# Kernel tuning notes

Hardware: AMD Instinct MI355X
Metric: run time of the kernel (lower is better)

The kernel has to match this reference:

```python
import jax, jax.numpy as jnp
import numpy as np
from jax import lax

B, T, H, L, V = 64, 512, 1024, 4, 32000


def setup_inputs() -> dict:
    key = jax.random.key(0)
    ks = jax.random.split(key, 8)
    lengths = jax.random.randint(ks[0], (B,), T // 2, T + 1)
    tok = jax.random.randint(ks[1], (B, T), 1, V)  # valid tokens are >0; 0 is pad
    x = jnp.where(jnp.arange(T)[None, :] < lengths[:, None], tok, 0)
    s = float(1.0 / np.sqrt(H))  # torch LSTMCell default init bound
    emb = jax.random.normal(ks[2], (V, H), jnp.float32) * 0.02
    W_ih = jax.random.uniform(ks[3], (L, 4 * H, H), jnp.float32, -s, s)
    W_hh = jax.random.uniform(ks[4], (L, 4 * H, H), jnp.float32, -s, s)
    b_ih = jax.random.uniform(ks[5], (L, 4 * H), jnp.float32, -s, s)
    b_hh = jax.random.uniform(ks[6], (L, 4 * H), jnp.float32, -s, s)
    h0 = jnp.zeros((L, B, H), jnp.float32)
    c0 = jnp.zeros((L, B, H), jnp.float32)
    return {"x": x, "h0": h0, "c0": c0, "emb": emb,
            "W_ih": W_ih, "W_hh": W_hh, "b_ih": b_ih, "b_hh": b_hh}


def _lstm_stack_step(h, c, xt, W_ih, W_hh, b_ih, b_hh):
    # h, c: [L, B, H]; xt: [B, H]. Every layer is H->H (module quirk).
    inp = xt
    new_h, new_c = [], []
    for l in range(L):
        gates = inp @ W_ih[l].T + b_ih[l] + h[l] @ W_hh[l].T + b_hh[l]  # [B, 4H]
        i, f, g, o = jnp.split(gates, 4, axis=-1)  # torch gate order i,f,g,o
        i = jax.nn.sigmoid(i)
        f = jax.nn.sigmoid(f)
        g = jnp.tanh(g)
        o = jax.nn.sigmoid(o)
        cl = f * c[l] + i * g
        hl = o * jnp.tanh(cl)
        new_h.append(hl)
        new_c.append(cl)
        inp = hl
    return jnp.stack(new_h), jnp.stack(new_c)


def reference(x, h0, c0, emb, W_ih, W_hh, b_ih, b_hh):
    # lengths from pad-token convention (pad id = 0)
    lengths = jnp.sum(x > 0, axis=1)  # [B]
    # pack(..., enforce_sorted=False): sort sequences by length, descending.
    order = jnp.argsort(-lengths)          # stable descending sort
    inv = jnp.argsort(order)               # to unsort the padded output
    xs = x[order]                          # [B, T] sorted order
    lens = lengths[order]                  # [B]
    e = emb[xs]                            # [B, T, H] embedded
    mask = jnp.arange(T)[None, :] < lens[:, None]  # [B, T] active-at-step

    def step(carry, inp):
        h, c = carry                       # [L, B, H] each
        xt, m = inp                        # xt: [B, H], m: [B] bool
        nh, nc = _lstm_stack_step(h, c, xt, W_ih, W_hh, b_ih, b_hh)
        m3 = m[None, :, None]
        h2 = jnp.where(m3, nh, h)          # only active (prefix) rows advance
        c2 = jnp.where(m3, nc, c)
        out = jnp.where(m[:, None], nh[L - 1], 0.0)  # unpack zero-pads
        return (h2, c2), out

    (hF, cF), outs = lax.scan(step, (h0, c0),
                              (jnp.swapaxes(e, 0, 1), mask.T))  # scan over T
    output = jnp.swapaxes(outs, 0, 1)[inv]  # [B, T, H] back to original order
    # NOTE: the torch module returns `state` indexed in SORTED order (it never
    # unsorts the state buffer); we reproduce that quirk faithfully.
    return output, hF, cF
```

## Files before the change

### kernel.cpp

```cpp
#include <hip/hip_runtime.h>
#include <hip/hip_bf16.h>
#include <stdint.h>

#define Bn 64
#define Tn 512
#define Hn 1024
#define Ln 4
#define GN 4096
#define NDIAG (Tn + Ln - 1)
#define LBH (Ln * Bn * Hn)

typedef __attribute__((ext_vector_type(8))) short bf16x8;
typedef __attribute__((ext_vector_type(4))) float f32x4;
typedef __attribute__((ext_vector_type(4))) unsigned short u16x4;

__device__ __forceinline__ unsigned short f2bf(float f) {
  union { float f; unsigned u; } v; v.f = f;
  return (unsigned short)((v.u + 0x7FFFu + ((v.u >> 16) & 1u)) >> 16);
}

__device__ __forceinline__ void gload16(const void* g, void* l) {
  __builtin_amdgcn_global_load_lds((const __attribute__((address_space(1))) void*)g,
                                   (__attribute__((address_space(3))) void*)l, 16, 0, 0);
}
__device__ __forceinline__ void gload16c(const void* g, void* l) {
  __builtin_amdgcn_global_load_lds((const __attribute__((address_space(1))) void*)g,
                                   (__attribute__((address_space(3))) void*)l, 16, 0, 17);
}

__device__ __forceinline__ float sigmf(float x) { return 1.0f / (1.0f + expf(-x)); }

__global__ __launch_bounds__(256) void prep_kernel(const int* __restrict__ x, int* __restrict__ len,
                                                   int* __restrict__ rank, int* __restrict__ arr) {
  __shared__ int sl[Bn];
  int t = threadIdx.x;
  if (t < 4) arr[t] = 0;
  if (t < Bn) {
    int cnt = 0;
    const int* row = x + (size_t)t * Tn;
    for (int i = 0; i < Tn; ++i) cnt += (row[i] > 0) ? 1 : 0;
    sl[t] = cnt;
  }
  __syncthreads();
  if (t < Bn) {
    int Lb = sl[t], r = 0;
    for (int j = 0; j < Bn; ++j) {
      int lj = sl[j];
      r += ((lj > Lb) || (lj == Lb && j < t)) ? 1 : 0;
    }
    len[t] = Lb;
    rank[t] = r;
  }
}

__global__ void bias_kernel(const float* __restrict__ bih, const float* __restrict__ bhh,
                            float* __restrict__ bias) {
  int i = blockIdx.x * blockDim.x + threadIdx.x;
  if (i < Ln * GN) bias[i] = bih[i] + bhh[i];
}

__global__ __launch_bounds__(256) void cast_w_kernel(const float* __restrict__ Wih,
                                                     const float* __restrict__ Whh,
                                                     unsigned short* __restrict__ Wlay) {
  size_t i = (size_t)blockIdx.x * blockDim.x + threadIdx.x;
  int k4 = (int)(i & 511);
  int n  = (int)((i >> 9) & 4095);
  int l  = (int)(i >> 21);
  int bn = n >> 6, j = n & 63;
  int strip = j >> 4, hcl = j & 15;
  int g = strip * 1024 + bn * 16 + hcl;
  int k = k4 * 4;
  f32x4 v;
  if (k < 1024) v = *(const f32x4*)(Wih + ((size_t)l * GN + g) * Hn + k);
  else          v = *(const f32x4*)(Whh + ((size_t)l * GN + g) * Hn + (k - 1024));
  u16x4 pv;
#pragma unroll
  for (int u = 0; u < 4; ++u) pv[u] = f2bf(v[u]);
  *(u16x4*)(Wlay + i * 4) = pv;
}

__global__ __launch_bounds__(256) void embed_kernel(const int* __restrict__ x,
                                                    const float* __restrict__ emb,
                                                    unsigned short* __restrict__ Xemb) {
  int row = blockIdx.x;
  int t = row >> 6, b = row & 63;
  int tok = x[(size_t)b * Tn + t];
  f32x4 v = ((const f32x4*)(emb + (size_t)tok * Hn))[threadIdx.x];
  u16x4 p;
#pragma unroll
  for (int u = 0; u < 4; ++u) p[u] = f2bf(v[u]);
  ((u16x4*)(Xemb + (size_t)row * Hn))[threadIdx.x] = p;
}

__global__ __launch_bounds__(256) void init_hmask_kernel(const float* __restrict__ h0,
                                                         unsigned short* __restrict__ hmask) {
  int i = blockIdx.x * blockDim.x + threadIdx.x;
  unsigned short us = f2bf(h0[i]);
#pragma unroll
  for (int dep = 0; dep < 4; ++dep)
    hmask[(size_t)dep * LBH + i] = us;
}

__device__ __forceinline__ void stage2(const char* inb, const char* hmb, int ph, char* buf,
                                       int tid, bool cohIn) {
#pragma unroll
  for (int j = 0; j < 2; ++j) {
    int o = j * 8192 + tid * 16;
    int row = o >> 8, win = o & 255;
    int sw = win ^ ((row & 15) << 4);
    const char* s1 = inb + (size_t)row * 2048 + ph * 256 + sw;
    if (cohIn) gload16c(s1, buf + o);
    else       gload16(s1, buf + o);
    gload16c(hmb + (size_t)row * 2048 + ph * 256 + sw, buf + 16384 + o);
  }
}

__global__ __launch_bounds__(512, 2) void wavefront_kernel(
    const char* __restrict__ Wlay, const float* __restrict__ biasF,
    const char* __restrict__ Xemb,
    unsigned short* __restrict__ hmask, unsigned short* __restrict__ hfresh,
    const int* __restrict__ len, const int* __restrict__ rankp,
    const float* __restrict__ h0, const float* __restrict__ c0,
    float* __restrict__ outp, float* __restrict__ hF, float* __restrict__ cF,
    int* __restrict__ arr) {
  __shared__ char smem[98304];
  int tid = threadIdx.x, bid = blockIdx.x;
  int cell = (bid & 7) >> 1;
  int bn = (bid & 1) * 32 + (bid >> 3);
  int w = tid >> 6, lane = tid & 63, l15 = lane & 15, lk = lane >> 4;
  int kq = w >> 1, sp = w & 1;

  bf16x8 wreg[32];
#pragma unroll
  for (int st = 0; st < 2; ++st) {
    const char* wr = Wlay + ((size_t)((cell * 64 + bn) * 64 + (sp * 2 + st) * 16 + l15)) * 4096
                   + (kq >= 2 ? 2048 : 0) + (kq & 1) * 128 + lk * 16;
#pragma unroll
    for (int ph = 0; ph < 8; ++ph)
#pragma unroll
      for (int j = 0; j < 2; ++j)
        wreg[st * 16 + ph * 2 + j] = *(const bf16x8*)(wr + ph * 256 + j * 64);
  }

  int r = tid >> 2;
  int c0i = (tid & 3) << 2;
  int hc = bn * 16 + c0i;
  f32x4 bI = {}, bF = {}, bG = {}, bO = {}, hold = {}, cold = {};
  int lenr = 0, rnkr = 0;
  if (tid < 256) {
    const float* bias = biasF + cell * GN;
    bI = *(const f32x4*)(bias + hc);
    bF = *(const f32x4*)(bias + 1024 + hc);
    bG = *(const f32x4*)(bias + 2048 + hc);
    bO = *(const f32x4*)(bias + 3072 + hc);
    lenr = len[r];
    rnkr = rankp[r];
    hold = *(const f32x4*)(h0 + ((size_t)cell * Bn + r) * Hn + hc);
    cold = *(const f32x4*)(c0 + ((size_t)cell * Bn + r) * Hn + hc);
  }

  for (int d = 0; d < NDIAG; ++d) {
    int t = d - cell;
    if (t >= 0 && t < Tn) {
      if (tid == 0 && cell > 0) {
        int thr = 64 * d;
        while (__hip_atomic_load(&arr[cell - 1], __ATOMIC_RELAXED, __HIP_MEMORY_SCOPE_AGENT) < thr)
          __builtin_amdgcn_s_sleep(1);
      }
      if (tid == 1) {
        int thr = 64 * d;
        while (__hip_atomic_load(&arr[cell], __ATOMIC_RELAXED, __HIP_MEMORY_SCOPE_AGENT) < thr)
          __builtin_amdgcn_s_sleep(1);
      }
      if (tid == 2 && cell < Ln - 1 && d >= 2) {
        int thr = 64 * (d - 2);
        while (__hip_atomic_load(&arr[cell + 1], __ATOMIC_RELAXED, __HIP_MEMORY_SCOPE_AGENT) < thr)
          __builtin_amdgcn_s_sleep(1);
      }
      __syncthreads();

      bool cohIn = (cell != 0);
      const char* inbase = (cell == 0)
          ? (Xemb + (size_t)t * (Bn * Hn * 2))
          : (const char*)(hfresh + ((size_t)((d - 1) & 3) * Ln + (cell - 1)) * (Bn * Hn));
      const char* hmbase = (const char*)(hmask + ((size_t)((d - 1) & 3) * Ln + cell) * (Bn * Hn));
      unsigned short* hmW = hmask + ((size_t)(d & 3) * Ln + cell) * (Bn * Hn);
      unsigned short* hfW = hfresh + ((size_t)(d & 3) * Ln + cell) * (Bn * Hn);

      f32x4 acc[2][4] = {};
      stage2(inbase, hmbase, 0, smem, tid, cohIn);
      stage2(inbase, hmbase, 1, smem + 32768, tid, cohIn);
#pragma unroll
      for (int ph = 0; ph < 8; ++ph) {
        if (ph < 7) asm volatile("s_waitcnt vmcnt(4)" ::: "memory");
        else        asm volatile("s_waitcnt vmcnt(0)" ::: "memory");
        __builtin_amdgcn_s_barrier();
        if (ph < 6) stage2(inbase, hmbase, ph + 2, smem + ((ph + 2) % 3) * 32768, tid, cohIn);
        const char* chunk = smem + (ph % 3) * 32768 + (kq >= 2 ? 16384 : 0);
        int colb = (kq & 1) * 128;
#pragma unroll
        for (int j = 0; j < 2; ++j) {
#pragma unroll
          for (int mi = 0; mi < 4; ++mi) {
            int row = mi * 16 + l15;
            bf16x8 afr = *(const bf16x8*)(chunk + row * 256 +
                          ((colb + j * 64 + lk * 16) ^ ((row & 15) << 4)));
            acc[0][mi] = __builtin_amdgcn_mfma_f32_16x16x32_bf16(afr, wreg[ph * 2 + j],
                                                                 acc[0][mi], 0, 0, 0);
            acc[1][mi] = __builtin_amdgcn_mfma_f32_16x16x32_bf16(afr, wreg[16 + ph * 2 + j],
                                                                 acc[1][mi], 0, 0, 0);
          }
        }
      }

#pragma unroll
      for (int st = 0; st < 2; ++st) {
        int ri = kq * 4 + (sp * 2 + st);
        float* exf = (float*)(smem + (ri < 8 ? ri * 4096 : 32768 + ri * 4096));
#pragma unroll
        for (int mi = 0; mi < 4; ++mi)
#pragma unroll
          for (int j = 0; j < 4; ++j)
            exf[(mi * 16 + lk * 4 + j) * 16 + l15] = acc[st][mi][j];
      }
      __syncthreads();

      if (tid < 256) {
        f32x4 sv[4];
#pragma unroll
        for (int g = 0; g < 4; ++g) {
          f32x4 s = {};
#pragma unroll
          for (int q = 0; q < 4; ++q) {
            int ri = q * 4 + g;
            const float* exf = (const float*)(smem + (ri < 8 ? ri * 4096 : 32768 + ri * 4096));
            f32x4 v = *(const f32x4*)(exf + r * 16 + c0i);
#pragma unroll
            for (int u = 0; u < 4; ++u) s[u] += v[u];
          }
          sv[g] = s;
        }
        bool msk = (t < lenr);
        f32x4 hx;
#pragma unroll
        for (int u = 0; u < 4; ++u) {
          float iv = sigmf(sv[0][u] + bI[u]);
          float fv = sigmf(sv[1][u] + bF[u]);
          float gv = tanhf(sv[2][u] + bG[u]);
          float ov = sigmf(sv[3][u] + bO[u]);
          float cc = fv * cold[u] + iv * gv;
          float hh = ov * tanhf(cc);
          hx[u] = hh;
          cold[u] = msk ? cc : cold[u];
          hold[u] = msk ? hh : hold[u];
        }
        unsigned hb01 = (unsigned)f2bf(hold[0]) | ((unsigned)f2bf(hold[1]) << 16);
        unsigned hb23 = (unsigned)f2bf(hold[2]) | ((unsigned)f2bf(hold[3]) << 16);
        unsigned xb01 = (unsigned)f2bf(hx[0]) | ((unsigned)f2bf(hx[1]) << 16);
        unsigned xb23 = (unsigned)f2bf(hx[2]) | ((unsigned)f2bf(hx[3]) << 16);
        unsigned* hm32 = (unsigned*)(hmW + (size_t)r * Hn + hc);
        unsigned* hf32p = (unsigned*)(hfW + (size_t)r * Hn + hc);
        __hip_atomic_store(hm32,     hb01, __ATOMIC_RELAXED, __HIP_MEMORY_SCOPE_AGENT);
        __hip_atomic_store(hm32 + 1, hb23, __ATOMIC_RELAXED, __HIP_MEMORY_SCOPE_AGENT);
        __hip_atomic_store(hf32p,     xb01, __ATOMIC_RELAXED, __HIP_MEMORY_SCOPE_AGENT);
        __hip_atomic_store(hf32p + 1, xb23, __ATOMIC_RELAXED, __HIP_MEMORY_SCOPE_AGENT);
        if (cell == Ln - 1) {
          f32x4 o4;
#pragma unroll
          for (int u = 0; u < 4; ++u) o4[u] = msk ? hx[u] : 0.0f;
          *(f32x4*)(outp + ((size_t)r * Tn + t) * Hn + hc) = o4;
        }
      }
    }

    __syncthreads();
    if (tid == 0)
      __hip_atomic_fetch_add(&arr[cell], 1, __ATOMIC_RELAXED, __HIP_MEMORY_SCOPE_AGENT);
  }

  if (tid < 256) {
    *(f32x4*)(hF + ((size_t)cell * Bn + rnkr) * Hn + hc) = hold;
    *(f32x4*)(cF + ((size_t)cell * Bn + rnkr) * Hn + hc) = cold;
  }
}

extern "C" void kernel_launch(void* const* d_in, const int* in_sizes, int n_in,
                              void* d_out, int out_size, void* d_ws, size_t ws_size,
                              hipStream_t stream) {
  const int*   x   = (const int*)d_in[0];
  const float* h0  = (const float*)d_in[1];
  const float* c0  = (const float*)d_in[2];
  const float* emb = (const float*)d_in[3];
  const float* Wih = (const float*)d_in[4];
  const float* Whh = (const float*)d_in[5];
  const float* bih = (const float*)d_in[6];
  const float* bhh = (const float*)d_in[7];
  float* out = (float*)d_out;

  char* ws = (char*)d_ws;
  unsigned short* Wlay  = (unsigned short*)ws;
  float*          biasF = (float*)(ws + 67108864);
  unsigned short* Xemb  = (unsigned short*)(ws + 67174400);
  unsigned short* hmask = (unsigned short*)(ws + 134283264);
  unsigned short* hfresh= (unsigned short*)(ws + 136380416);
  int*            leni  = (int*)(ws + 138477568);
  int*            ranki = (int*)(ws + 138477824);
  int*            arrp  = (int*)(ws + 138478080);

  prep_kernel<<<1, 256, 0, stream>>>(x, leni, ranki, arrp);
  bias_kernel<<<64, 256, 0, stream>>>(bih, bhh, biasF);
  cast_w_kernel<<<32768, 256, 0, stream>>>(Wih, Whh, Wlay);
  embed_kernel<<<Tn * Bn, 256, 0, stream>>>(x, emb, Xemb);
  init_hmask_kernel<<<1024, 256, 0, stream>>>(h0, hmask);

  float* hFbase = out + (size_t)Bn * Tn * Hn;
  float* cFbase = hFbase + (size_t)Ln * Bn * Hn;

  wavefront_kernel<<<256, 512, 0, stream>>>(
      (const char*)Wlay, biasF, (const char*)Xemb, hmask, hfresh,
      leni, ranki, h0, c0, out, hFbase, cFbase, arrp);
}
```

Baseline: 5.629 ms.

## Replace shared atomic counters with per-block progress flags and acquire fence

Each layer's single fetch-add counter is replaced by a per-block progress slot (64 per layer), written with a plain atomic store. A whole wavefront polls the 64 slots in parallel and uses a wave vote to wait. The cache-coherent (glc/slc) LDS-direct loads are replaced by ordinary loads, with an agent-scope acquire fence after the wait standing in for them. The aim is to remove contention on a single atomic line and the cost of uncached loads. The trade-off is an extra barrier per step and reliance on the fence for memory visibility.

```diff
diff --git a/kernel.cpp b/kernel.cpp
--- a/kernel.cpp
+++ b/kernel.cpp
@@ -23,10 +23,6 @@
   __builtin_amdgcn_global_load_lds((const __attribute__((address_space(1))) void*)g,
                                    (__attribute__((address_space(3))) void*)l, 16, 0, 0);
 }
-__device__ __forceinline__ void gload16c(const void* g, void* l) {
-  __builtin_amdgcn_global_load_lds((const __attribute__((address_space(1))) void*)g,
-                                   (__attribute__((address_space(3))) void*)l, 16, 0, 17);
-}
 
 __device__ __forceinline__ float sigmf(float x) { return 1.0f / (1.0f + expf(-x)); }
 
@@ -34,7 +30,7 @@
                                                    int* __restrict__ rank, int* __restrict__ arr) {
   __shared__ int sl[Bn];
   int t = threadIdx.x;
-  if (t < 4) arr[t] = 0;
+  arr[t] = 0;
   if (t < Bn) {
     int cnt = 0;
     const int* row = x + (size_t)t * Tn;
@@ -101,17 +97,14 @@
     hmask[(size_t)dep * LBH + i] = us;
 }
 
-__device__ __forceinline__ void stage2(const char* inb, const char* hmb, int ph, char* buf,
-                                       int tid, bool cohIn) {
+__device__ __forceinline__ void stage2(const char* inb, const char* hmb, int ph, char* buf, int tid) {
 #pragma unroll
   for (int j = 0; j < 2; ++j) {
     int o = j * 8192 + tid * 16;
     int row = o >> 8, win = o & 255;
     int sw = win ^ ((row & 15) << 4);
-    const char* s1 = inb + (size_t)row * 2048 + ph * 256 + sw;
-    if (cohIn) gload16c(s1, buf + o);
-    else       gload16(s1, buf + o);
-    gload16c(hmb + (size_t)row * 2048 + ph * 256 + sw, buf + 16384 + o);
+    gload16(inb + (size_t)row * 2048 + ph * 256 + sw, buf + o);
+    gload16(hmb + (size_t)row * 2048 + ph * 256 + sw, buf + 16384 + o);
   }
 }
 
@@ -162,24 +155,34 @@
   for (int d = 0; d < NDIAG; ++d) {
     int t = d - cell;
     if (t >= 0 && t < Tn) {
-      if (tid == 0 && cell > 0) {
-        int thr = 64 * d;
-        while (__hip_atomic_load(&arr[cell - 1], __ATOMIC_RELAXED, __HIP_MEMORY_SCOPE_AGENT) < thr)
+      if (w == 0 && cell > 0) {
+        for (;;) {
+          int v = __hip_atomic_load(&arr[(cell - 1) * 64 + lane], __ATOMIC_RELAXED,
+                                    __HIP_MEMORY_SCOPE_AGENT);
+          if (__all(v >= d)) break;
           __builtin_amdgcn_s_sleep(1);
-      }
-      if (tid == 1) {
-        int thr = 64 * d;
-        while (__hip_atomic_load(&arr[cell], __ATOMIC_RELAXED, __HIP_MEMORY_SCOPE_AGENT) < thr)
+        }
+      }
+      if (w == 1) {
+        for (;;) {
+          int v = __hip_atomic_load(&arr[cell * 64 + lane], __ATOMIC_RELAXED,
+                                    __HIP_MEMORY_SCOPE_AGENT);
+          if (__all(v >= d)) break;
           __builtin_amdgcn_s_sleep(1);
-      }
-      if (tid == 2 && cell < Ln - 1 && d >= 2) {
-        int thr = 64 * (d - 2);
-        while (__hip_atomic_load(&arr[cell + 1], __ATOMIC_RELAXED, __HIP_MEMORY_SCOPE_AGENT) < thr)
+        }
+      }
+      if (w == 2 && cell < Ln - 1 && d >= 2) {
+        for (;;) {
+          int v = __hip_atomic_load(&arr[(cell + 1) * 64 + lane], __ATOMIC_RELAXED,
+                                    __HIP_MEMORY_SCOPE_AGENT);
+          if (__all(v >= d - 2)) break;
           __builtin_amdgcn_s_sleep(1);
+        }
       }
       __syncthreads();
-
-      bool cohIn = (cell != 0);
+      if (tid == 0) __builtin_amdgcn_fence(__ATOMIC_ACQUIRE, "agent");
+      __syncthreads();
+
       const char* inbase = (cell == 0)
           ? (Xemb + (size_t)t * (Bn * Hn * 2))
           : (const char*)(hfresh + ((size_t)((d - 1) & 3) * Ln + (cell - 1)) * (Bn * Hn));
@@ -188,14 +191,14 @@
       unsigned short* hfW = hfresh + ((size_t)(d & 3) * Ln + cell) * (Bn * Hn);
 
       f32x4 acc[2][4] = {};
-      stage2(inbase, hmbase, 0, smem, tid, cohIn);
-      stage2(inbase, hmbase, 1, smem + 32768, tid, cohIn);
+      stage2(inbase, hmbase, 0, smem, tid);
+      stage2(inbase, hmbase, 1, smem + 32768, tid);
 #pragma unroll
       for (int ph = 0; ph < 8; ++ph) {
         if (ph < 7) asm volatile("s_waitcnt vmcnt(4)" ::: "memory");
         else        asm volatile("s_waitcnt vmcnt(0)" ::: "memory");
         __builtin_amdgcn_s_barrier();
-        if (ph < 6) stage2(inbase, hmbase, ph + 2, smem + ((ph + 2) % 3) * 32768, tid, cohIn);
+        if (ph < 6) stage2(inbase, hmbase, ph + 2, smem + ((ph + 2) % 3) * 32768, tid);
         const char* chunk = smem + (ph % 3) * 32768 + (kq >= 2 ? 16384 : 0);
         int colb = (kq & 1) * 128;
 #pragma unroll
@@ -275,7 +278,7 @@
 
     __syncthreads();
     if (tid == 0)
-      __hip_atomic_fetch_add(&arr[cell], 1, __ATOMIC_RELAXED, __HIP_MEMORY_SCOPE_AGENT);
+      __hip_atomic_store(&arr[cell * 64 + bn], d + 1, __ATOMIC_RELAXED, __HIP_MEMORY_SCOPE_AGENT);
   }
 
   if (tid < 256) {
```

New measurement: 5.170 ms. 8.2% less time.
